# Performance work log

Hardware: AMD Instinct MI355X
Metric: run time of the kernel (lower is better)

## Reference

```python
import jax, jax.numpy as jnp
import numpy as np

D_MODEL = 2048
NUM_Q_HEADS = 32
NUM_KV_HEADS = 8
HEAD_DIM = D_MODEL // NUM_Q_HEADS  # 64
NUM_GROUPS = NUM_Q_HEADS // NUM_KV_HEADS  # 4


def setup_inputs() -> dict:
    key = jax.random.key(0)
    ks = jax.random.split(key, 9)
    s = 1.0 / np.sqrt(D_MODEL)
    x = jax.random.normal(ks[0], (2, 2048, D_MODEL), dtype=jnp.float32)
    Wq = jax.random.uniform(ks[1], (D_MODEL, NUM_Q_HEADS * HEAD_DIM), jnp.float32, -s, s)
    bq = jax.random.uniform(ks[2], (NUM_Q_HEADS * HEAD_DIM,), jnp.float32, -s, s)
    Wk = jax.random.uniform(ks[3], (D_MODEL, NUM_KV_HEADS * HEAD_DIM), jnp.float32, -s, s)
    bk = jax.random.uniform(ks[4], (NUM_KV_HEADS * HEAD_DIM,), jnp.float32, -s, s)
    Wv = jax.random.uniform(ks[5], (D_MODEL, NUM_KV_HEADS * HEAD_DIM), jnp.float32, -s, s)
    bv = jax.random.uniform(ks[6], (NUM_KV_HEADS * HEAD_DIM,), jnp.float32, -s, s)
    Wo = jax.random.uniform(ks[7], (D_MODEL, D_MODEL), jnp.float32, -s, s)
    bo = jax.random.uniform(ks[8], (D_MODEL,), jnp.float32, -s, s)
    return {"x": x, "Wq": Wq, "bq": bq, "Wk": Wk, "bk": bk,
            "Wv": Wv, "bv": bv, "Wo": Wo, "bo": bo}


def reference(x, Wq, bq, Wk, bk, Wv, bv, Wo, bo):
    B, T, C = x.shape
    Hkv, G, Dh = NUM_KV_HEADS, NUM_GROUPS, HEAD_DIM
    # projections
    q = (x @ Wq + bq).reshape(B, T, Hkv, G, Dh)   # group G query heads per kv head
    k = (x @ Wk + bk).reshape(B, T, Hkv, Dh)
    v = (x @ Wv + bv).reshape(B, T, Hkv, Dh)
    scale = 1.0 / np.sqrt(Dh).astype(np.float32)
    # scores: [B, Hkv, G, T, T] (kv head broadcast over its G query heads)
    scores = jnp.einsum('btkgd,bskd->bkgts', q, k) * scale
    attn = jax.nn.softmax(scores, axis=-1)
    out = jnp.einsum('bkgts,bskd->btkgd', attn, v).reshape(B, T, C)
    return out @ Wo + bo
```

## Files before the change

### kernel.cpp

```cpp
#include <hip/hip_runtime.h>
#include <cstdint>
#include <cstddef>
#include <math.h>

typedef uint16_t bf16;
typedef __attribute__((ext_vector_type(8))) __bf16 bf16x8;
typedef __attribute__((ext_vector_type(2))) float f32x2;
typedef __attribute__((ext_vector_type(4))) float f32x4;
typedef __attribute__((ext_vector_type(16))) float f32x16;

#define MFMA16(a,b,c) __builtin_amdgcn_mfma_f32_16x16x32_bf16((a),(b),(c),0,0,0)
#define MFMA32(a,b,c) __builtin_amdgcn_mfma_f32_32x32x16_bf16((a),(b),(c),0,0,0)

__device__ __forceinline__ uint16_t f2bf(float f){
  uint32_t u = __float_as_uint(f);
  return (uint16_t)((u + 0x7fffu + ((u >> 16) & 1u)) >> 16);
}
__device__ __forceinline__ uint32_t pk2(float lo, float hi){
  return (uint32_t)f2bf(lo) | ((uint32_t)f2bf(hi) << 16);
}

__device__ __forceinline__ void gload_lds16(const void* g, void* l){
  __builtin_amdgcn_global_load_lds((const __attribute__((address_space(1))) void*)g,
                                   (__attribute__((address_space(3))) void*)l, 16, 0, 0);
}

__global__ void k_convert(const float* __restrict__ in, bf16* __restrict__ out, int n){
  int i = (blockIdx.x * 256 + threadIdx.x) * 4;
  if (i >= n) return;
  float4 v = *reinterpret_cast<const float4*>(in + i);
  uint32_t lo = pk2(v.x, v.y);
  uint32_t hi = pk2(v.z, v.w);
  uint2 pkv = make_uint2(lo, hi);
  *reinterpret_cast<uint2*>(out + i) = pkv;
}

__global__ void k_transposeW(const float* __restrict__ in, bf16* __restrict__ out, int R, int C){
  __shared__ float tile[32][33];
  int c0 = blockIdx.x * 32, r0 = blockIdx.y * 32;
  int tx = threadIdx.x, ty = threadIdx.y;
  #pragma unroll
  for (int i = 0; i < 4; i++)
    tile[ty + 8*i][tx] = in[(size_t)(r0 + ty + 8*i) * C + c0 + tx];
  __syncthreads();
  #pragma unroll
  for (int i = 0; i < 4; i++)
    out[(size_t)(c0 + ty + 8*i) * R + r0 + tx] = f2bf(tile[tx][ty + 8*i]);
}

__global__ void k_transposeV(const bf16* __restrict__ v, bf16* __restrict__ vt){
  __shared__ bf16 tile[32][33];
  int c0 = blockIdx.x * 32, r0 = blockIdx.y * 32;
  int tx = threadIdx.x, ty = threadIdx.y;
  #pragma unroll
  for (int i = 0; i < 4; i++)
    tile[ty + 8*i][tx] = v[(size_t)(r0 + ty + 8*i) * 512 + c0 + tx];
  __syncthreads();
  int b = r0 >> 11; int t0 = r0 & 2047;
  #pragma unroll
  for (int i = 0; i < 4; i++)
    vt[((size_t)b * 512 + c0 + ty + 8*i) * 2048 + t0 + tx] = tile[tx][ty + 8*i];
}

__device__ __forceinline__ void gemm128_core(
    const bf16* __restrict__ Abase, const bf16* __restrict__ Btbase,
    int lda, int ldb, int K, bf16* As, bf16* Bs, f32x4 acc[4][4])
{
  const int tid = threadIdx.x;
  const int wid = tid >> 6, lane = tid & 63;
  const int wr = wid >> 1, wc = wid & 1;
  const int lr = lane & 15, lg = lane >> 4;
  const f32x4 vzero = {0.f, 0.f, 0.f, 0.f};

  #pragma unroll
  for (int m = 0; m < 4; m++)
    #pragma unroll
    for (int n = 0; n < 4; n++)
      acc[m][n] = vzero;

  int srcA[4], srcB[4], dOff[4];
  #pragma unroll
  for (int i = 0; i < 4; i++){
    int d = i*4096 + wid*1024 + lane*16;
    int row = d >> 7, sp = (d >> 4) & 7;
    int sl = sp ^ (row & 7);
    srcA[i] = row * lda + sl * 8;
    srcB[i] = row * ldb + sl * 8;
    dOff[i] = i*4096 + wid*1024;
  }

  for (int k0 = 0; k0 < K; k0 += 64){
    #pragma unroll
    for (int i = 0; i < 4; i++)
      gload_lds16(Abase + k0 + srcA[i], (char*)As + dOff[i]);
    #pragma unroll
    for (int i = 0; i < 4; i++)
      gload_lds16(Btbase + k0 + srcB[i], (char*)Bs + dOff[i]);
    __syncthreads();
    #pragma unroll
    for (int ks = 0; ks < 2; ks++){
      bf16x8 af[4], bfr[4];
      #pragma unroll
      for (int m = 0; m < 4; m++){
        int row = wr*64 + m*16 + lr;
        int sp = (ks*4 + lg) ^ (row & 7);
        af[m] = *reinterpret_cast<const bf16x8*>(As + row*64 + sp*8);
      }
      #pragma unroll
      for (int n = 0; n < 4; n++){
        int row = wc*64 + n*16 + lr;
        int sp = (ks*4 + lg) ^ (row & 7);
        bfr[n] = *reinterpret_cast<const bf16x8*>(Bs + row*64 + sp*8);
      }
      #pragma unroll
      for (int m = 0; m < 4; m++)
        #pragma unroll
        for (int n = 0; n < 4; n++)
          acc[m][n] = MFMA16(af[m], bfr[n], acc[m][n]);
    }
    __syncthreads();
  }
}

__global__ __launch_bounds__(256, 2) void k_qkv(
    const bf16* __restrict__ xb,
    const bf16* __restrict__ WqT, const bf16* __restrict__ WkT, const bf16* __restrict__ WvT,
    const float* __restrict__ bq, const float* __restrict__ bk, const float* __restrict__ bv,
    bf16* __restrict__ qo, bf16* __restrict__ ko, bf16* __restrict__ vo)
{
  __shared__ __align__(16) bf16 As[128*64];
  __shared__ __align__(16) bf16 Bs[128*64];
  int by = blockIdx.y;
  const bf16* Bt; const float* bias; bf16* outp; int ldc; float scale;
  if (by < 16){      Bt = WqT + (size_t)by*128*2048;      bias = bq + by*128;      outp = qo + by*128;      ldc = 2048; scale = 0.18033688011112042f; }
  else if (by < 20){ int y = by-16; Bt = WkT + (size_t)y*128*2048; bias = bk + y*128; outp = ko + y*128; ldc = 512;  scale = 1.f; }
  else {             int y = by-20; Bt = WvT + (size_t)y*128*2048; bias = bv + y*128; outp = vo + y*128; ldc = 512;  scale = 1.f; }
  int m0 = blockIdx.x * 128;
  f32x4 acc[4][4];
  gemm128_core(xb + (size_t)m0*2048, Bt, 2048, 2048, 2048, As, Bs, acc);
  const int tid = threadIdx.x, wid = tid >> 6, lane = tid & 63;
  const int wr = wid >> 1, wc = wid & 1, lr = lane & 15, lg = lane >> 4;
  #pragma unroll
  for (int n = 0; n < 4; n++){
    int col = wc*64 + n*16 + lr;
    float bb = bias[col];
    #pragma unroll
    for (int m = 0; m < 4; m++)
      #pragma unroll
      for (int r = 0; r < 4; r++){
        int row = m0 + wr*64 + m*16 + lg*4 + r;
        outp[(size_t)row*ldc + col] = f2bf((acc[m][n][r] + bb) * scale);
      }
  }
}

__global__ __launch_bounds__(256, 2) void k_oproj(
    const bf16* __restrict__ ab, const bf16* __restrict__ WoT,
    const float* __restrict__ bo, float* __restrict__ outp)
{
  __shared__ __align__(16) bf16 As[128*64];
  __shared__ __align__(16) bf16 Bs[128*64];
  int m0 = blockIdx.x * 128, n0 = blockIdx.y * 128;
  f32x4 acc[4][4];
  gemm128_core(ab + (size_t)m0*2048, WoT + (size_t)n0*2048, 2048, 2048, 2048, As, Bs, acc);
  const int tid = threadIdx.x, wid = tid >> 6, lane = tid & 63;
  const int wr = wid >> 1, wc = wid & 1, lr = lane & 15, lg = lane >> 4;
  #pragma unroll
  for (int n = 0; n < 4; n++){
    int col = n0 + wc*64 + n*16 + lr;
    float bb = bo[col];
    #pragma unroll
    for (int m = 0; m < 4; m++)
      #pragma unroll
      for (int r = 0; r < 4; r++){
        int row = m0 + wr*64 + m*16 + lg*4 + r;
        outp[(size_t)row*2048 + col] = acc[m][n][r] + bb;
      }
  }
}

__global__ __launch_bounds__(512, 4) void k_flash(
    const bf16* __restrict__ q, const bf16* __restrict__ kmat,
    const bf16* __restrict__ vt, bf16* __restrict__ ao)
{
  __shared__ __align__(16) bf16 Ks[2][128*64];
  __shared__ __align__(16) bf16 Vs[2][64*128];
  const int tid = threadIdx.x;
  const int wid = tid >> 6, lane = tid & 63;
  const int l31 = lane & 31, hi = lane >> 5;
  const int bh = blockIdx.y;
  const int b = bh >> 5, hq = bh & 31, kvh = hq >> 2;
  const int qt = blockIdx.x;
  const int qrow0 = b*2048 + qt*256 + wid*32;

  bf16x8 qf[4];
  {
    const bf16* qrow = q + (size_t)(qrow0 + l31)*2048 + hq*64 + hi*8;
    #pragma unroll
    for (int t = 0; t < 4; t++)
      qf[t] = *reinterpret_cast<const bf16x8*>(qrow + t*16);
  }

  f32x16 oacc[2];
  #pragma unroll
  for (int n = 0; n < 2; n++)
    #pragma unroll
    for (int r = 0; r < 16; r++) oacc[n][r] = 0.f;
  f32x2 rp[4];
  #pragma unroll
  for (int j = 0; j < 4; j++){ rp[j][0] = 0.f; rp[j][1] = 0.f; }
  const f32x16 zv = {0.f,0.f,0.f,0.f,0.f,0.f,0.f,0.f,0.f,0.f,0.f,0.f,0.f,0.f,0.f,0.f};

  const bf16* kbase = kmat + (size_t)b*2048*512 + kvh*64;
  const bf16* vbase = vt + ((size_t)b*512 + kvh*64)*2048;

  int kSrc[2], vSrc[2], dOff[2];
  #pragma unroll
  for (int i = 0; i < 2; i++){
    int db = i*8192 + tid*16;
    int krow = db >> 7, ksp = (db >> 4) & 7,  ksl = ksp ^ (krow & 7);
    int vrow = db >> 8, vsp = (db >> 4) & 15, vsl = vsp ^ (vrow & 7);
    kSrc[i] = krow*512  + ksl*8;
    vSrc[i] = vrow*2048 + vsl*8;
    dOff[i] = i*8192 + wid*1024;
  }

  #define STAGE(buf, st_) do { \
    const bf16* kb_ = kbase + (size_t)(st_)*128*512; \
    const bf16* vb_ = vbase + (st_)*128; \
    gload_lds16(kb_ + kSrc[0], (char*)Ks[buf] + dOff[0]); \
    gload_lds16(kb_ + kSrc[1], (char*)Ks[buf] + dOff[1]); \
    gload_lds16(vb_ + vSrc[0], (char*)Vs[buf] + dOff[0]); \
    gload_lds16(vb_ + vSrc[1], (char*)Vs[buf] + dOff[1]); \
  } while(0)

  STAGE(0, 0);
  __syncthreads();

  for (int st = 0; st < 16; st++){
    int cur = st & 1;
    if (st < 15) STAGE(cur^1, st+1);

    #pragma unroll
    for (int c = 0; c < 2; c++){
      f32x16 sc[2];
      __builtin_amdgcn_s_setprio(1);
      {
        bf16x8 af[2];
        #pragma unroll
        for (int n = 0; n < 2; n++){
          int row = 64*c + 32*n + l31;
          int ph = hi ^ (row & 7);
          af[n] = *reinterpret_cast<const bf16x8*>(Ks[cur] + row*64 + ph*8);
        }
        #pragma unroll
        for (int n = 0; n < 2; n++)
          sc[n] = MFMA32(af[n], qf[0], zv);
      }
      #pragma unroll
      for (int t = 1; t < 4; t++){
        bf16x8 af[2];
        #pragma unroll
        for (int n = 0; n < 2; n++){
          int row = 64*c + 32*n + l31;
          int ph = (2*t + hi) ^ (row & 7);
          af[n] = *reinterpret_cast<const bf16x8*>(Ks[cur] + row*64 + ph*8);
        }
        #pragma unroll
        for (int n = 0; n < 2; n++)
          sc[n] = MFMA32(af[n], qf[t], sc[n]);
      }
      __builtin_amdgcn_s_setprio(0);

      uint32_t pw[2][8];
      #pragma unroll
      for (int n = 0; n < 2; n++)
        #pragma unroll
        for (int j = 0; j < 8; j++){
          float plo = __builtin_amdgcn_exp2f(sc[n][2*j]);
          float phi = __builtin_amdgcn_exp2f(sc[n][2*j+1]);
          f32x2 e; e[0] = plo; e[1] = phi;
          rp[j & 3] += e;
          asm("v_cvt_pk_bf16_f32 %0, %1, %2" : "=v"(pw[n][j]) : "v"(plo), "v"(phi));
        }
      #pragma unroll
      for (int n = 0; n < 2; n++)
        #pragma unroll
        for (int h = 0; h < 2; h++){
          asm volatile("v_permlane32_swap_b32 %0, %1" : "+v"(pw[n][h*4+0]), "+v"(pw[n][h*4+2]));
          asm volatile("v_permlane32_swap_b32 %0, %1" : "+v"(pw[n][h*4+1]), "+v"(pw[n][h*4+3]));
        }

      __builtin_amdgcn_s_setprio(1);
      #pragma unroll
      for (int kk = 0; kk < 4; kk++){
        int n = kk >> 1, h = kk & 1;
        union { uint32_t w[4]; bf16x8 v; } pa;
        pa.w[0] = pw[n][h*4+0]; pa.w[1] = pw[n][h*4+1];
        pa.w[2] = pw[n][h*4+2]; pa.w[3] = pw[n][h*4+3];
        bf16x8 vf[2];
        #pragma unroll
        for (int nd = 0; nd < 2; nd++){
          int row = 32*nd + l31;
          int ph = (8*c + 2*kk + hi) ^ (row & 7);
          vf[nd] = *reinterpret_cast<const bf16x8*>(Vs[cur] + row*128 + ph*8);
        }
        #pragma unroll
        for (int nd = 0; nd < 2; nd++)
          oacc[nd] = MFMA32(pa.v, vf[nd], oacc[nd]);
      }
      __builtin_amdgcn_s_setprio(0);
    }
    __syncthreads();
  }
  #undef STAGE

  float rs = (rp[0][0] + rp[0][1]) + (rp[1][0] + rp[1][1])
           + (rp[2][0] + rp[2][1]) + (rp[3][0] + rp[3][1]);
  float l = rs + __shfl_xor(rs, 32);
  float linv = 1.f / l;
  float lv[16];
  #pragma unroll
  for (int r = 0; r < 16; r++){
    int qi = (r & 3) + 8*(r >> 2) + 4*hi;
    lv[r] = __shfl(linv, qi);
  }
  #pragma unroll
  for (int nd = 0; nd < 2; nd++)
    #pragma unroll
    for (int r = 0; r < 16; r++){
      int qi = (r & 3) + 8*(r >> 2) + 4*hi;
      int row = qrow0 + qi;
      ao[(size_t)row*2048 + hq*64 + nd*32 + l31] = f2bf(oacc[nd][r] * lv[r]);
    }
}

extern "C" void kernel_launch(void* const* d_in, const int* in_sizes, int n_in,
                              void* d_out, int out_size, void* d_ws, size_t ws_size,
                              hipStream_t stream)
{
  const float* x  = (const float*)d_in[0];
  const float* Wq = (const float*)d_in[1];
  const float* bq = (const float*)d_in[2];
  const float* Wk = (const float*)d_in[3];
  const float* bk = (const float*)d_in[4];
  const float* Wv = (const float*)d_in[5];
  const float* bv = (const float*)d_in[6];
  const float* Wo = (const float*)d_in[7];
  const float* bo = (const float*)d_in[8];
  float* out = (float*)d_out;

  char* ws = (char*)d_ws;
  size_t off = 0;
  auto alloc = [&](size_t bytes){ char* p = ws + off; off += (bytes + 255) & ~(size_t)255; return p; };
  bf16* xb  = (bf16*)alloc(2*2048*2048*2);
  bf16* WqT = (bf16*)alloc(2048*2048*2);
  bf16* WkT = (bf16*)alloc(512*2048*2);
  bf16* WvT = (bf16*)alloc(512*2048*2);
  bf16* WoT = (bf16*)alloc(2048*2048*2);
  bf16* qb  = (bf16*)alloc(4096*2048*2);
  bf16* kb  = (bf16*)alloc((size_t)4096*512*2);
  bf16* vb  = (bf16*)alloc((size_t)4096*512*2);
  bf16* vtb = (bf16*)alloc((size_t)4096*512*2);
  bf16* aob = xb;

  k_convert<<<8192, 256, 0, stream>>>(x, xb, 2*2048*2048);
  k_transposeW<<<dim3(64,64), dim3(32,8), 0, stream>>>(Wq, WqT, 2048, 2048);
  k_transposeW<<<dim3(16,64), dim3(32,8), 0, stream>>>(Wk, WkT, 2048, 512);
  k_transposeW<<<dim3(16,64), dim3(32,8), 0, stream>>>(Wv, WvT, 2048, 512);
  k_transposeW<<<dim3(64,64), dim3(32,8), 0, stream>>>(Wo, WoT, 2048, 2048);
  k_qkv<<<dim3(32,24), 256, 0, stream>>>(xb, WqT, WkT, WvT, bq, bk, bv, qb, kb, vb);
  k_transposeV<<<dim3(16,128), dim3(32,8), 0, stream>>>(vb, vtb);
  k_flash<<<dim3(8,64), 512, 0, stream>>>(qb, kb, vtb, aob);
  k_oproj<<<dim3(32,16), 256, 0, stream>>>(aob, WoT, bo, out);
}
```

Measured before the change: 199.5 us.

## Fuse V transpose into QKV epilogue, vectorize weight transpose, simplify flash LDS addressing

The QKV projection kernel now writes V directly in transposed layout, which removes the separate V transpose kernel and the intermediate V buffer. The weight transpose kernel uses 64x64 tiles with float4 loads and 16-byte packed bf16 stores instead of scalar accesses. The flash kernel uses a single LDS buffer with precomputed per-lane swizzled offsets, toggled by XOR between stages, and a new V tile layout, to cut address arithmetic in the inner loop. In exchange, the transposed V stores from the QKV epilogue are 8-byte strided writes that may coalesce poorly, and the new V LDS layout must stay consistent with the staging pattern.

```diff
diff --git a/kernel.cpp b/kernel.cpp
--- a/kernel.cpp
+++ b/kernel.cpp
@@ -36,30 +36,28 @@
 }
 
 __global__ void k_transposeW(const float* __restrict__ in, bf16* __restrict__ out, int R, int C){
-  __shared__ float tile[32][33];
-  int c0 = blockIdx.x * 32, r0 = blockIdx.y * 32;
-  int tx = threadIdx.x, ty = threadIdx.y;
-  #pragma unroll
-  for (int i = 0; i < 4; i++)
-    tile[ty + 8*i][tx] = in[(size_t)(r0 + ty + 8*i) * C + c0 + tx];
+  __shared__ float tile[64][65];
+  int c0 = blockIdx.x * 64, r0 = blockIdx.y * 64;
+  int t = threadIdx.x;
+  int fx = t & 15, fy = t >> 4;
+  #pragma unroll
+  for (int i = 0; i < 4; i++){
+    int r = fy + i*16;
+    float4 v = *reinterpret_cast<const float4*>(in + (size_t)(r0 + r)*C + c0 + fx*4);
+    tile[r][fx*4+0] = v.x; tile[r][fx*4+1] = v.y;
+    tile[r][fx*4+2] = v.z; tile[r][fx*4+3] = v.w;
+  }
   __syncthreads();
-  #pragma unroll
-  for (int i = 0; i < 4; i++)
-    out[(size_t)(c0 + ty + 8*i) * R + r0 + tx] = f2bf(tile[tx][ty + 8*i]);
-}
-
-__global__ void k_transposeV(const bf16* __restrict__ v, bf16* __restrict__ vt){
-  __shared__ bf16 tile[32][33];
-  int c0 = blockIdx.x * 32, r0 = blockIdx.y * 32;
-  int tx = threadIdx.x, ty = threadIdx.y;
-  #pragma unroll
-  for (int i = 0; i < 4; i++)
-    tile[ty + 8*i][tx] = v[(size_t)(r0 + ty + 8*i) * 512 + c0 + tx];
-  __syncthreads();
-  int b = r0 >> 11; int t0 = r0 & 2047;
-  #pragma unroll
-  for (int i = 0; i < 4; i++)
-    vt[((size_t)b * 512 + c0 + ty + 8*i) * 2048 + t0 + tx] = tile[tx][ty + 8*i];
+  int gx = t & 7, gy = t >> 3;
+  #pragma unroll
+  for (int i = 0; i < 2; i++){
+    int c = gy + i*32;
+    int rr = gx*8;
+    union { bf16 h[8]; uint4 u; } pk_;
+    #pragma unroll
+    for (int j = 0; j < 8; j++) pk_.h[j] = f2bf(tile[rr+j][c]);
+    *reinterpret_cast<uint4*>(out + (size_t)(c0 + c)*R + r0 + rr) = pk_.u;
+  }
 }
 
 __device__ __forceinline__ void gemm128_core(
@@ -126,31 +124,50 @@
     const bf16* __restrict__ xb,
     const bf16* __restrict__ WqT, const bf16* __restrict__ WkT, const bf16* __restrict__ WvT,
     const float* __restrict__ bq, const float* __restrict__ bk, const float* __restrict__ bv,
-    bf16* __restrict__ qo, bf16* __restrict__ ko, bf16* __restrict__ vo)
+    bf16* __restrict__ qo, bf16* __restrict__ ko, bf16* __restrict__ vtp)
 {
   __shared__ __align__(16) bf16 As[128*64];
   __shared__ __align__(16) bf16 Bs[128*64];
   int by = blockIdx.y;
-  const bf16* Bt; const float* bias; bf16* outp; int ldc; float scale;
-  if (by < 16){      Bt = WqT + (size_t)by*128*2048;      bias = bq + by*128;      outp = qo + by*128;      ldc = 2048; scale = 0.18033688011112042f; }
-  else if (by < 20){ int y = by-16; Bt = WkT + (size_t)y*128*2048; bias = bk + y*128; outp = ko + y*128; ldc = 512;  scale = 1.f; }
-  else {             int y = by-20; Bt = WvT + (size_t)y*128*2048; bias = bv + y*128; outp = vo + y*128; ldc = 512;  scale = 1.f; }
+  const bf16* Bt; const float* bias; int mode; int y = 0; float scale = 1.f;
+  if (by < 16){      Bt = WqT + (size_t)by*128*2048;      bias = bq + by*128; mode = 0; y = by;   scale = 0.18033688011112042f; }
+  else if (by < 20){ y = by-16; Bt = WkT + (size_t)y*128*2048; bias = bk + y*128; mode = 1; }
+  else {             y = by-20; Bt = WvT + (size_t)y*128*2048; bias = bv + y*128; mode = 2; }
   int m0 = blockIdx.x * 128;
   f32x4 acc[4][4];
   gemm128_core(xb + (size_t)m0*2048, Bt, 2048, 2048, 2048, As, Bs, acc);
   const int tid = threadIdx.x, wid = tid >> 6, lane = tid & 63;
   const int wr = wid >> 1, wc = wid & 1, lr = lane & 15, lg = lane >> 4;
-  #pragma unroll
-  for (int n = 0; n < 4; n++){
-    int col = wc*64 + n*16 + lr;
-    float bb = bias[col];
-    #pragma unroll
-    for (int m = 0; m < 4; m++)
-      #pragma unroll
-      for (int r = 0; r < 4; r++){
-        int row = m0 + wr*64 + m*16 + lg*4 + r;
-        outp[(size_t)row*ldc + col] = f2bf((acc[m][n][r] + bb) * scale);
-      }
+  if (mode == 2){
+    #pragma unroll
+    for (int n = 0; n < 4; n++){
+      int cl = wc*64 + n*16 + lr;
+      float bb = bias[cl];
+      #pragma unroll
+      for (int m = 0; m < 4; m++){
+        int row0 = m0 + wr*64 + m*16 + lg*4;
+        int bi = row0 >> 11, tl = row0 & 2047;
+        union { bf16 h[4]; uint2 u; } pk_;
+        #pragma unroll
+        for (int r = 0; r < 4; r++) pk_.h[r] = f2bf(acc[m][n][r] + bb);
+        *reinterpret_cast<uint2*>(vtp + ((size_t)bi*512 + y*128 + cl)*2048 + tl) = pk_.u;
+      }
+    }
+  } else {
+    bf16* outp = (mode == 0) ? (qo + y*128) : (ko + y*128);
+    int ldc = (mode == 0) ? 2048 : 512;
+    #pragma unroll
+    for (int n = 0; n < 4; n++){
+      int col = wc*64 + n*16 + lr;
+      float bb = bias[col];
+      #pragma unroll
+      for (int m = 0; m < 4; m++)
+        #pragma unroll
+        for (int r = 0; r < 4; r++){
+          int row = m0 + wr*64 + m*16 + lg*4 + r;
+          outp[(size_t)row*ldc + col] = f2bf((acc[m][n][r] + bb) * scale);
+        }
+    }
   }
 }
 
@@ -183,8 +200,7 @@
     const bf16* __restrict__ q, const bf16* __restrict__ kmat,
     const bf16* __restrict__ vt, bf16* __restrict__ ao)
 {
-  __shared__ __align__(16) bf16 Ks[2][128*64];
-  __shared__ __align__(16) bf16 Vs[2][64*128];
+  __shared__ __align__(16) char lds[65536];
   const int tid = threadIdx.x;
   const int wid = tid >> 6, lane = tid & 63;
   const int l31 = lane & 31, hi = lane >> 5;
@@ -211,65 +227,58 @@
   for (int j = 0; j < 4; j++){ rp[j][0] = 0.f; rp[j][1] = 0.f; }
   const f32x16 zv = {0.f,0.f,0.f,0.f,0.f,0.f,0.f,0.f,0.f,0.f,0.f,0.f,0.f,0.f,0.f,0.f};
 
+  const int r7 = l31 & 7;
+  int A[8];
+  #pragma unroll
+  for (int j = 0; j < 8; j++)
+    A[j] = l31*128 + (((2*j + hi) ^ r7) << 4);
+
   const bf16* kbase = kmat + (size_t)b*2048*512 + kvh*64;
   const bf16* vbase = vt + ((size_t)b*512 + kvh*64)*2048;
 
-  int kSrc[2], vSrc[2], dOff[2];
+  int kSrc[2], vSrc[2];
+  const int dOf = wid*1024;
   #pragma unroll
   for (int i = 0; i < 2; i++){
-    int db = i*8192 + tid*16;
-    int krow = db >> 7, ksp = (db >> 4) & 7,  ksl = ksp ^ (krow & 7);
-    int vrow = db >> 8, vsp = (db >> 4) & 15, vsl = vsp ^ (vrow & 7);
-    kSrc[i] = krow*512  + ksl*8;
-    vSrc[i] = vrow*2048 + vsl*8;
-    dOff[i] = i*8192 + wid*1024;
+    int kdb = i*8192 + tid*16;
+    int krow = kdb >> 7, ksp = (kdb >> 4) & 7, ksl = ksp ^ (krow & 7);
+    kSrc[i] = krow*512 + ksl*8;
+    int o = tid*16;
+    int vrow = o >> 7, vsp = (o >> 4) & 7, vsl = vsp ^ (vrow & 7);
+    vSrc[i] = vrow*2048 + i*64 + vsl*8;
   }
 
   #define STAGE(buf, st_) do { \
     const bf16* kb_ = kbase + (size_t)(st_)*128*512; \
     const bf16* vb_ = vbase + (st_)*128; \
-    gload_lds16(kb_ + kSrc[0], (char*)Ks[buf] + dOff[0]); \
-    gload_lds16(kb_ + kSrc[1], (char*)Ks[buf] + dOff[1]); \
-    gload_lds16(vb_ + vSrc[0], (char*)Vs[buf] + dOff[0]); \
-    gload_lds16(vb_ + vSrc[1], (char*)Vs[buf] + dOff[1]); \
+    gload_lds16(kb_ + kSrc[0], lds + (buf)*16384 + dOf); \
+    gload_lds16(kb_ + kSrc[1], lds + (buf)*16384 + 8192 + dOf); \
+    gload_lds16(vb_ + vSrc[0], lds + 32768 + (buf)*16384 + dOf); \
+    gload_lds16(vb_ + vSrc[1], lds + 32768 + (buf)*16384 + 8192 + dOf); \
   } while(0)
+
+  #define LDK(j, imm) (*reinterpret_cast<const bf16x8*>(lds + A[j] + (imm)))
+  #define LDV(j, imm) (*reinterpret_cast<const bf16x8*>(lds + A[j] + 32768 + (imm)))
 
   STAGE(0, 0);
   __syncthreads();
 
+  int cur = 0;
   for (int st = 0; st < 16; st++){
-    int cur = st & 1;
     if (st < 15) STAGE(cur^1, st+1);
 
     #pragma unroll
     for (int c = 0; c < 2; c++){
       f32x16 sc[2];
       __builtin_amdgcn_s_setprio(1);
-      {
-        bf16x8 af[2];
-        #pragma unroll
-        for (int n = 0; n < 2; n++){
-          int row = 64*c + 32*n + l31;
-          int ph = hi ^ (row & 7);
-          af[n] = *reinterpret_cast<const bf16x8*>(Ks[cur] + row*64 + ph*8);
-        }
+      #pragma unroll
+      for (int n = 0; n < 2; n++)
+        sc[n] = MFMA32(LDK(0, c*8192 + n*4096), qf[0], zv);
+      #pragma unroll
+      for (int t = 1; t < 4; t++)
         #pragma unroll
         for (int n = 0; n < 2; n++)
-          sc[n] = MFMA32(af[n], qf[0], zv);
-      }
-      #pragma unroll
-      for (int t = 1; t < 4; t++){
-        bf16x8 af[2];
-        #pragma unroll
-        for (int n = 0; n < 2; n++){
-          int row = 64*c + 32*n + l31;
-          int ph = (2*t + hi) ^ (row & 7);
-          af[n] = *reinterpret_cast<const bf16x8*>(Ks[cur] + row*64 + ph*8);
-        }
-        #pragma unroll
-        for (int n = 0; n < 2; n++)
-          sc[n] = MFMA32(af[n], qf[t], sc[n]);
-      }
+          sc[n] = MFMA32(LDK(t, c*8192 + n*4096), qf[t], sc[n]);
       __builtin_amdgcn_s_setprio(0);
 
       uint32_t pw[2][8];
@@ -298,22 +307,20 @@
         union { uint32_t w[4]; bf16x8 v; } pa;
         pa.w[0] = pw[n][h*4+0]; pa.w[1] = pw[n][h*4+1];
         pa.w[2] = pw[n][h*4+2]; pa.w[3] = pw[n][h*4+3];
-        bf16x8 vf[2];
-        #pragma unroll
-        for (int nd = 0; nd < 2; nd++){
-          int row = 32*nd + l31;
-          int ph = (8*c + 2*kk + hi) ^ (row & 7);
-          vf[nd] = *reinterpret_cast<const bf16x8*>(Vs[cur] + row*128 + ph*8);
-        }
         #pragma unroll
         for (int nd = 0; nd < 2; nd++)
-          oacc[nd] = MFMA32(pa.v, vf[nd], oacc[nd]);
+          oacc[nd] = MFMA32(pa.v, LDV(kk, c*8192 + nd*4096), oacc[nd]);
       }
       __builtin_amdgcn_s_setprio(0);
     }
     __syncthreads();
+    #pragma unroll
+    for (int j = 0; j < 8; j++) A[j] ^= 16384;
+    cur ^= 1;
   }
   #undef STAGE
+  #undef LDK
+  #undef LDV
 
   float rs = (rp[0][0] + rp[0][1]) + (rp[1][0] + rp[1][1])
            + (rp[2][0] + rp[2][1]) + (rp[3][0] + rp[3][1]);
@@ -360,17 +367,15 @@
   bf16* WoT = (bf16*)alloc(2048*2048*2);
   bf16* qb  = (bf16*)alloc(4096*2048*2);
   bf16* kb  = (bf16*)alloc((size_t)4096*512*2);
-  bf16* vb  = (bf16*)alloc((size_t)4096*512*2);
   bf16* vtb = (bf16*)alloc((size_t)4096*512*2);
   bf16* aob = xb;
 
   k_convert<<<8192, 256, 0, stream>>>(x, xb, 2*2048*2048);
-  k_transposeW<<<dim3(64,64), dim3(32,8), 0, stream>>>(Wq, WqT, 2048, 2048);
-  k_transposeW<<<dim3(16,64), dim3(32,8), 0, stream>>>(Wk, WkT, 2048, 512);
-  k_transposeW<<<dim3(16,64), dim3(32,8), 0, stream>>>(Wv, WvT, 2048, 512);
-  k_transposeW<<<dim3(64,64), dim3(32,8), 0, stream>>>(Wo, WoT, 2048, 2048);
-  k_qkv<<<dim3(32,24), 256, 0, stream>>>(xb, WqT, WkT, WvT, bq, bk, bv, qb, kb, vb);
-  k_transposeV<<<dim3(16,128), dim3(32,8), 0, stream>>>(vb, vtb);
+  k_transposeW<<<dim3(32,32), 256, 0, stream>>>(Wq, WqT, 2048, 2048);
+  k_transposeW<<<dim3(8,32),  256, 0, stream>>>(Wk, WkT, 2048, 512);
+  k_transposeW<<<dim3(8,32),  256, 0, stream>>>(Wv, WvT, 2048, 512);
+  k_transposeW<<<dim3(32,32), 256, 0, stream>>>(Wo, WoT, 2048, 2048);
+  k_qkv<<<dim3(32,24), 256, 0, stream>>>(xb, WqT, WkT, WvT, bq, bk, bv, qb, kb, vtb);
   k_flash<<<dim3(8,64), 512, 0, stream>>>(qb, kb, vtb, aob);
   k_oproj<<<dim3(32,16), 256, 0, stream>>>(aob, WoT, bo, out);
 }
```

After: 195.0 us. 2.2% less time.
